# Performance work log

Measured on AMD Instinct MI355X. Metric: run time of the kernel, lower is better.

The kernel has to match this reference:

```python
import jax, jax.numpy as jnp
import numpy as np

B, T, K = 1024, 512, 64  # batch, max_seq_len, num_tags


def setup_inputs() -> dict:
    key = jax.random.key(0)
    k1, k2, k3, k4 = jax.random.split(key, 4)
    logits = jax.random.normal(k1, (B, T, K), dtype=jnp.float32)
    trans = jax.random.normal(k2, (K, K), dtype=jnp.float32) * 0.1  # self._crf_weights
    gold = jax.random.randint(k3, (B, T), 0, K)
    # training sentences contain at least 2 words (per the assignment comment)
    seq_len = jax.random.randint(k4, (B,), 2, T + 1)
    return {"logits": logits, "trans": trans, "gold": gold, "seq_len": seq_len}


def reference(logits, trans, gold, seq_len):
    # crf_loss: loss = -crf_log_likelihood(...) / batch_size
    Bsz, Tlen, _ = logits.shape
    pos = jnp.arange(Tlen)
    valid = pos[None, :] < seq_len[:, None]  # [B, T]

    # first_loss: sum of unary scores at gold tags over valid positions
    unary = jnp.take_along_axis(logits, gold[..., None], axis=2)[..., 0]  # [B, T]
    first = jnp.sum(jnp.where(valid, unary, 0.0))

    # second_loss: sum of transition scores trans[gold_t, gold_{t+1}] for t+1 < seq_len
    pair = trans[gold[:, :-1], gold[:, 1:]]  # [B, T-1]
    valid_pair = pos[None, :-1] < (seq_len - 1)[:, None]
    second = jnp.sum(jnp.where(valid_pair, pair, 0.0))

    # third_loss: log-partition via forward recurrence
    # alpha_new[a] = logsumexp_b(trans[a, b] + alpha[b]) + logits[:, t, a]
    # (note: source reduces over axis=1 of (trans + alpha), i.e. the second index)
    def step(alpha, xs):
        t, lt = xs  # lt: [B, K] logits at time t
        new = jax.nn.logsumexp(trans[None, :, :] + alpha[:, None, :], axis=2) + lt
        alpha = jnp.where((t < seq_len)[:, None], new, alpha)
        return alpha, None

    alpha0 = logits[:, 0, :]                         # [B, K]
    ts = jnp.arange(1, Tlen)
    rest = jnp.swapaxes(logits[:, 1:, :], 0, 1)      # [T-1, B, K]
    alpha_final, _ = jax.lax.scan(step, alpha0, (ts, rest))
    third = jnp.sum(jax.nn.logsumexp(alpha_final, axis=1))

    log_like = first + second - third
    return -log_like / Bsz
```

## Files before the change

kernel.cpp:

```cpp
#include <hip/hip_runtime.h>

#define BB 1024
#define TT 512
#define KK 64
#define CH 8

typedef _Float16 f16x2 __attribute__((ext_vector_type(2)));
typedef float f32x4 __attribute__((ext_vector_type(4)));
typedef unsigned int u32x4 __attribute__((ext_vector_type(4)));

__device__ __forceinline__ float wave_sum(float v) {
#pragma unroll
    for (int off = 1; off < 64; off <<= 1) v += __shfl_xor(v, off);
    return v;
}

__device__ __forceinline__ float wave_max(float v) {
#pragma unroll
    for (int off = 1; off < 64; off <<= 1) v = fmaxf(v, __shfl_xor(v, off));
    return v;
}

#if __has_builtin(__builtin_amdgcn_fdot2)
#define FDOT2(E, P, A) __builtin_amdgcn_fdot2((E), (P), (A), false)
#else
__device__ __forceinline__ float fdot2_emul(f16x2 e, f16x2 p, float a) {
    return fmaf((float)e.x, (float)p.x, fmaf((float)e.y, (float)p.y, a));
}
#define FDOT2(E, P, A) fdot2_emul((E), (P), (A))
#endif

__global__ void __launch_bounds__(64)
__attribute__((amdgpu_waves_per_eu(1, 1)))
crf_fwd(
    const float* __restrict__ logits,
    const float* __restrict__ trans,
    const int* __restrict__ gold,
    const int* __restrict__ seq_len,
    float* __restrict__ ws)
{
    __shared__ __align__(16) _Float16 plds[KK];
    const int b = blockIdx.x;
    const int j = threadIdx.x & 63;
    const float* lg = logits + (size_t)b * (TT * KK);
    const int* gd = gold + (size_t)b * TT;
    const int L = seq_len[b];

    float af = 0.0f, asec = 0.0f;
#pragma unroll
    for (int c = 0; c < TT / 64; ++c) {
        int t = c * 64 + j;
        if (t < L) {
            int g0 = gd[t];
            af += lg[t * KK + g0];
            if (t + 1 < L) {
                int g1 = gd[t + 1];
                asec += trans[g0 * KK + g1];
            }
        }
    }

    const float* Ej = trans + (size_t)j * KK;
#define DECLE(q) f16x2 Eh##q; { \
    float e0 = __expf(Ej[2 * (q)]); float e1 = __expf(Ej[2 * (q) + 1]); \
    Eh##q.x = (_Float16)e0; Eh##q.y = (_Float16)e1; }
    DECLE(0)  DECLE(1)  DECLE(2)  DECLE(3)  DECLE(4)  DECLE(5)  DECLE(6)  DECLE(7)
    DECLE(8)  DECLE(9)  DECLE(10) DECLE(11) DECLE(12) DECLE(13) DECLE(14) DECLE(15)
    DECLE(16) DECLE(17) DECLE(18) DECLE(19) DECLE(20) DECLE(21) DECLE(22) DECLE(23)
    DECLE(24) DECLE(25) DECLE(26) DECLE(27) DECLE(28) DECLE(29) DECLE(30) DECLE(31)
#undef DECLE

    float a0 = lg[j];
    float mx = wave_max(a0);
    float p0 = __expf(a0 - mx);
    _Float16 h0 = (_Float16)p0;
    float pq = (float)h0;
    plds[j] = h0;
    int Etot = 0;

    f32x4 nl0, nl1;
    nl0.x = lg[1 * KK + j]; nl0.y = lg[2 * KK + j];
    nl0.z = lg[3 * KK + j]; nl0.w = lg[4 * KK + j];
    nl1.x = lg[5 * KK + j]; nl1.y = lg[6 * KK + j];
    nl1.z = lg[7 * KK + j]; nl1.w = lg[8 * KK + j];

#define DOTQ(q, W, A) A = FDOT2(Eh##q, __builtin_bit_cast(f16x2, (W)), A);

#define STEP(ii, EL) { \
    const u32x4* pl4 = (const u32x4*)plds; \
    u32x4 R0 = pl4[0], R1 = pl4[1], R2 = pl4[2], R3 = pl4[3]; \
    u32x4 R4 = pl4[4], R5 = pl4[5], R6 = pl4[6], R7 = pl4[7]; \
    float A0 = 0.f, A1 = 0.f, A2 = 0.f, A3 = 0.f; \
    DOTQ(0,  R0.x, A0) DOTQ(1,  R0.y, A1) DOTQ(2,  R0.z, A2) DOTQ(3,  R0.w, A3) \
    DOTQ(4,  R1.x, A0) DOTQ(5,  R1.y, A1) DOTQ(6,  R1.z, A2) DOTQ(7,  R1.w, A3) \
    DOTQ(8,  R2.x, A0) DOTQ(9,  R2.y, A1) DOTQ(10, R2.z, A2) DOTQ(11, R2.w, A3) \
    DOTQ(12, R3.x, A0) DOTQ(13, R3.y, A1) DOTQ(14, R3.z, A2) DOTQ(15, R3.w, A3) \
    DOTQ(16, R4.x, A0) DOTQ(17, R4.y, A1) DOTQ(18, R4.z, A2) DOTQ(19, R4.w, A3) \
    DOTQ(20, R5.x, A0) DOTQ(21, R5.y, A1) DOTQ(22, R5.z, A2) DOTQ(23, R5.w, A3) \
    DOTQ(24, R6.x, A0) DOTQ(25, R6.y, A1) DOTQ(26, R6.z, A2) DOTQ(27, R6.w, A3) \
    DOTQ(28, R7.x, A0) DOTQ(29, R7.y, A1) DOTQ(30, R7.z, A2) DOTQ(31, R7.w, A3) \
    float s = (A0 + A1) + (A2 + A3); \
    float pn = s * (EL); \
    bool ok = (t0 + (ii)) < L; \
    pn = ok ? pn : pq; \
    unsigned sb = (unsigned)__builtin_amdgcn_readfirstlane((int)__float_as_uint(pn)); \
    int ee = ok ? ((int)((sb >> 23) & 255u) - 127) : 0; \
    Etot += ee; \
    float scl = __uint_as_float((unsigned)(127 - ee) << 23); \
    float qv = pn * scl; \
    _Float16 hq = (_Float16)qv; \
    pq = (float)hq; \
    plds[j] = hq; }

    for (int t0 = 1; t0 < L; t0 += CH) {
        asm volatile("" : "+v"(Eh0),  "+v"(Eh1),  "+v"(Eh2),  "+v"(Eh3),
                          "+v"(Eh4),  "+v"(Eh5),  "+v"(Eh6),  "+v"(Eh7),
                          "+v"(Eh8),  "+v"(Eh9),  "+v"(Eh10), "+v"(Eh11),
                          "+v"(Eh12), "+v"(Eh13), "+v"(Eh14), "+v"(Eh15));
        asm volatile("" : "+v"(Eh16), "+v"(Eh17), "+v"(Eh18), "+v"(Eh19),
                          "+v"(Eh20), "+v"(Eh21), "+v"(Eh22), "+v"(Eh23),
                          "+v"(Eh24), "+v"(Eh25), "+v"(Eh26), "+v"(Eh27),
                          "+v"(Eh28), "+v"(Eh29), "+v"(Eh30), "+v"(Eh31));

        f32x4 el0, el1;
        el0.x = __expf(nl0.x); el0.y = __expf(nl0.y);
        el0.z = __expf(nl0.z); el0.w = __expf(nl0.w);
        el1.x = __expf(nl1.x); el1.y = __expf(nl1.y);
        el1.z = __expf(nl1.z); el1.w = __expf(nl1.w);

        {
            int tn = t0 + CH;
            int c0 = tn + 0; c0 = (c0 > TT - 1) ? TT - 1 : c0;
            int c1 = tn + 1; c1 = (c1 > TT - 1) ? TT - 1 : c1;
            int c2 = tn + 2; c2 = (c2 > TT - 1) ? TT - 1 : c2;
            int c3 = tn + 3; c3 = (c3 > TT - 1) ? TT - 1 : c3;
            int c4 = tn + 4; c4 = (c4 > TT - 1) ? TT - 1 : c4;
            int c5 = tn + 5; c5 = (c5 > TT - 1) ? TT - 1 : c5;
            int c6 = tn + 6; c6 = (c6 > TT - 1) ? TT - 1 : c6;
            int c7 = tn + 7; c7 = (c7 > TT - 1) ? TT - 1 : c7;
            nl0.x = lg[c0 * KK + j]; nl0.y = lg[c1 * KK + j];
            nl0.z = lg[c2 * KK + j]; nl0.w = lg[c3 * KK + j];
            nl1.x = lg[c4 * KK + j]; nl1.y = lg[c5 * KK + j];
            nl1.z = lg[c6 * KK + j]; nl1.w = lg[c7 * KK + j];
        }

        STEP(0, el0.x) STEP(1, el0.y) STEP(2, el0.z) STEP(3, el0.w)
        STEP(4, el1.x) STEP(5, el1.y) STEP(6, el1.z) STEP(7, el1.w)
    }
#undef STEP
#undef DOTQ

    float sump = wave_sum(pq);
    float third_b = mx + (float)Etot * 0.6931471805599453f + __logf(sump);
    float first_b = wave_sum(af);
    float second_b = wave_sum(asec);

    if (j == 0) {
        ws[b] = (third_b - first_b - second_b) * (1.0f / (float)BB);
    }
}

__global__ void crf_reduce(const float* __restrict__ ws, float* __restrict__ out) {
    int tid = threadIdx.x;
    float v = ws[tid] + ws[tid + 256] + ws[tid + 512] + ws[tid + 768];
    v = wave_sum(v);
    __shared__ float sm[4];
    if ((tid & 63) == 0) sm[tid >> 6] = v;
    __syncthreads();
    if (tid == 0) out[0] = (sm[0] + sm[1]) + (sm[2] + sm[3]);
}

extern "C" void kernel_launch(void* const* d_in, const int* in_sizes, int n_in,
                              void* d_out, int out_size, void* d_ws, size_t ws_size,
                              hipStream_t stream) {
    const float* logits = (const float*)d_in[0];
    const float* trans  = (const float*)d_in[1];
    const int*   gold   = (const int*)d_in[2];
    const int*   slen   = (const int*)d_in[3];
    float* out = (float*)d_out;
    float* ws = (float*)d_ws;

    hipLaunchKernelGGL(crf_fwd, dim3(BB), dim3(64), 0, stream,
                       logits, trans, gold, slen, ws);
    hipLaunchKernelGGL(crf_reduce, dim3(1), dim3(256), 0, stream, ws, out);
}
```

Baseline: 103.6 us.

## Split matvec across lane quads with DPP reduction and peel the tail loop

Each lane now holds exp(trans) for four rows restricted to a 16-column slice, so each step reads only 32 bytes of the shared state vector instead of all 128. The per-row partial sums are combined across each quad of lanes with DPP xor-1 and xor-2 moves, replacing the previous full-row dot product per lane. The main loop now handles only full chunks of 8 steps, and a separate guarded tail handles the rest, which drops the per-step validity select and the register copy of the state. The aim is to cut LDS read traffic on the serial recurrence, at the cost of added cross-lane ops and select instructions on the critical path.

```diff
diff --git a/kernel.cpp b/kernel.cpp
--- a/kernel.cpp
+++ b/kernel.cpp
@@ -28,6 +28,20 @@
     return fmaf((float)e.x, (float)p.x, fmaf((float)e.y, (float)p.y, a));
 }
 #define FDOT2(E, P, A) fdot2_emul((E), (P), (A))
+#endif
+
+#if __has_builtin(__builtin_amdgcn_mov_dpp)
+__device__ __forceinline__ float dpp_xor1_f(float x) {
+    return __uint_as_float((unsigned)__builtin_amdgcn_mov_dpp(
+        (int)__float_as_uint(x), 0xB1, 0xF, 0xF, true));
+}
+__device__ __forceinline__ float dpp_xor2_f(float x) {
+    return __uint_as_float((unsigned)__builtin_amdgcn_mov_dpp(
+        (int)__float_as_uint(x), 0x4E, 0xF, 0xF, true));
+}
+#else
+__device__ __forceinline__ float dpp_xor1_f(float x) { return __shfl_xor(x, 1); }
+__device__ __forceinline__ float dpp_xor2_f(float x) { return __shfl_xor(x, 2); }
 #endif
 
 __global__ void __launch_bounds__(64)
@@ -46,6 +60,11 @@
     const int* gd = gold + (size_t)b * TT;
     const int L = seq_len[b];
 
+    const int quad_r = (j >> 2) << 2;
+    const int slice_c = (j & 3) << 4;
+    const bool lodd = (j & 1) != 0;
+    const bool lhi  = (j & 2) != 0;
+
     float af = 0.0f, asec = 0.0f;
 #pragma unroll
     for (int c = 0; c < TT / 64; ++c) {
@@ -60,22 +79,28 @@
         }
     }
 
-    const float* Ej = trans + (size_t)j * KK;
-#define DECLE(q) f16x2 Eh##q; { \
-    float e0 = __expf(Ej[2 * (q)]); float e1 = __expf(Ej[2 * (q) + 1]); \
-    Eh##q.x = (_Float16)e0; Eh##q.y = (_Float16)e1; }
-    DECLE(0)  DECLE(1)  DECLE(2)  DECLE(3)  DECLE(4)  DECLE(5)  DECLE(6)  DECLE(7)
-    DECLE(8)  DECLE(9)  DECLE(10) DECLE(11) DECLE(12) DECLE(13) DECLE(14) DECLE(15)
-    DECLE(16) DECLE(17) DECLE(18) DECLE(19) DECLE(20) DECLE(21) DECLE(22) DECLE(23)
-    DECLE(24) DECLE(25) DECLE(26) DECLE(27) DECLE(28) DECLE(29) DECLE(30) DECLE(31)
-#undef DECLE
+    f16x2 Eh0, Eh1, Eh2, Eh3, Eh4, Eh5, Eh6, Eh7;
+    f16x2 Eh8, Eh9, Eh10, Eh11, Eh12, Eh13, Eh14, Eh15;
+    f16x2 Eh16, Eh17, Eh18, Eh19, Eh20, Eh21, Eh22, Eh23;
+    f16x2 Eh24, Eh25, Eh26, Eh27, Eh28, Eh29, Eh30, Eh31;
+#define MKP(DST, a, bgt) { DST.x = (_Float16)__expf(a); DST.y = (_Float16)__expf(bgt); }
+#define DECROW(rr, N0, N1, N2, N3, N4, N5, N6, N7) { \
+    const float* row_ = trans + (size_t)(quad_r + (rr)) * KK + slice_c; \
+    f32x4 v0 = *(const f32x4*)(row_ + 0);  f32x4 v1 = *(const f32x4*)(row_ + 4); \
+    f32x4 v2 = *(const f32x4*)(row_ + 8);  f32x4 v3 = *(const f32x4*)(row_ + 12); \
+    MKP(N0, v0.x, v0.y) MKP(N1, v0.z, v0.w) MKP(N2, v1.x, v1.y) MKP(N3, v1.z, v1.w) \
+    MKP(N4, v2.x, v2.y) MKP(N5, v2.z, v2.w) MKP(N6, v3.x, v3.y) MKP(N7, v3.z, v3.w) }
+    DECROW(0, Eh0,  Eh1,  Eh2,  Eh3,  Eh4,  Eh5,  Eh6,  Eh7)
+    DECROW(1, Eh8,  Eh9,  Eh10, Eh11, Eh12, Eh13, Eh14, Eh15)
+    DECROW(2, Eh16, Eh17, Eh18, Eh19, Eh20, Eh21, Eh22, Eh23)
+    DECROW(3, Eh24, Eh25, Eh26, Eh27, Eh28, Eh29, Eh30, Eh31)
+#undef DECROW
+#undef MKP
 
     float a0 = lg[j];
     float mx = wave_max(a0);
     float p0 = __expf(a0 - mx);
-    _Float16 h0 = (_Float16)p0;
-    float pq = (float)h0;
-    plds[j] = h0;
+    plds[j] = (_Float16)p0;
     int Etot = 0;
 
     f32x4 nl0, nl1;
@@ -84,35 +109,38 @@
     nl1.x = lg[5 * KK + j]; nl1.y = lg[6 * KK + j];
     nl1.z = lg[7 * KK + j]; nl1.w = lg[8 * KK + j];
 
-#define DOTQ(q, W, A) A = FDOT2(Eh##q, __builtin_bit_cast(f16x2, (W)), A);
-
-#define STEP(ii, EL) { \
-    const u32x4* pl4 = (const u32x4*)plds; \
-    u32x4 R0 = pl4[0], R1 = pl4[1], R2 = pl4[2], R3 = pl4[3]; \
-    u32x4 R4 = pl4[4], R5 = pl4[5], R6 = pl4[6], R7 = pl4[7]; \
+    const u32x4* myslice = (const u32x4*)((const char*)plds + ((j & 3) << 5));
+
+#define DOTW(EH, W, A) A = FDOT2(EH, __builtin_bit_cast(f16x2, (W)), A);
+
+#define STEP(EL) { \
+    u32x4 Ra = myslice[0], Rb = myslice[1]; \
     float A0 = 0.f, A1 = 0.f, A2 = 0.f, A3 = 0.f; \
-    DOTQ(0,  R0.x, A0) DOTQ(1,  R0.y, A1) DOTQ(2,  R0.z, A2) DOTQ(3,  R0.w, A3) \
-    DOTQ(4,  R1.x, A0) DOTQ(5,  R1.y, A1) DOTQ(6,  R1.z, A2) DOTQ(7,  R1.w, A3) \
-    DOTQ(8,  R2.x, A0) DOTQ(9,  R2.y, A1) DOTQ(10, R2.z, A2) DOTQ(11, R2.w, A3) \
-    DOTQ(12, R3.x, A0) DOTQ(13, R3.y, A1) DOTQ(14, R3.z, A2) DOTQ(15, R3.w, A3) \
-    DOTQ(16, R4.x, A0) DOTQ(17, R4.y, A1) DOTQ(18, R4.z, A2) DOTQ(19, R4.w, A3) \
-    DOTQ(20, R5.x, A0) DOTQ(21, R5.y, A1) DOTQ(22, R5.z, A2) DOTQ(23, R5.w, A3) \
-    DOTQ(24, R6.x, A0) DOTQ(25, R6.y, A1) DOTQ(26, R6.z, A2) DOTQ(27, R6.w, A3) \
-    DOTQ(28, R7.x, A0) DOTQ(29, R7.y, A1) DOTQ(30, R7.z, A2) DOTQ(31, R7.w, A3) \
-    float s = (A0 + A1) + (A2 + A3); \
-    float pn = s * (EL); \
-    bool ok = (t0 + (ii)) < L; \
-    pn = ok ? pn : pq; \
+    float A4 = 0.f, A5 = 0.f, A6 = 0.f, A7 = 0.f; \
+    DOTW(Eh0,  Ra.x, A0) DOTW(Eh1,  Ra.y, A1) DOTW(Eh2,  Ra.z, A0) DOTW(Eh3,  Ra.w, A1) \
+    DOTW(Eh4,  Rb.x, A0) DOTW(Eh5,  Rb.y, A1) DOTW(Eh6,  Rb.z, A0) DOTW(Eh7,  Rb.w, A1) \
+    DOTW(Eh8,  Ra.x, A2) DOTW(Eh9,  Ra.y, A3) DOTW(Eh10, Ra.z, A2) DOTW(Eh11, Ra.w, A3) \
+    DOTW(Eh12, Rb.x, A2) DOTW(Eh13, Rb.y, A3) DOTW(Eh14, Rb.z, A2) DOTW(Eh15, Rb.w, A3) \
+    DOTW(Eh16, Ra.x, A4) DOTW(Eh17, Ra.y, A5) DOTW(Eh18, Ra.z, A4) DOTW(Eh19, Ra.w, A5) \
+    DOTW(Eh20, Rb.x, A4) DOTW(Eh21, Rb.y, A5) DOTW(Eh22, Rb.z, A4) DOTW(Eh23, Rb.w, A5) \
+    DOTW(Eh24, Ra.x, A6) DOTW(Eh25, Ra.y, A7) DOTW(Eh26, Ra.z, A6) DOTW(Eh27, Ra.w, A7) \
+    DOTW(Eh28, Rb.x, A6) DOTW(Eh29, Rb.y, A7) DOTW(Eh30, Rb.z, A6) DOTW(Eh31, Rb.w, A7) \
+    float P0 = A0 + A1, P1 = A2 + A3, P2 = A4 + A5, P3 = A6 + A7; \
+    float S0 = lodd ? P0 : P1, K0 = lodd ? P1 : P0; \
+    float S1 = lodd ? P2 : P3, K1 = lodd ? P3 : P2; \
+    float Q0 = K0 + dpp_xor1_f(S0); \
+    float Q1 = K1 + dpp_xor1_f(S1); \
+    float S2 = lhi ? Q0 : Q1, K2 = lhi ? Q1 : Q0; \
+    float s_ = K2 + dpp_xor2_f(S2); \
+    float pn = s_ * (EL); \
     unsigned sb = (unsigned)__builtin_amdgcn_readfirstlane((int)__float_as_uint(pn)); \
-    int ee = ok ? ((int)((sb >> 23) & 255u) - 127) : 0; \
+    int ee = (int)((sb >> 23) & 255u) - 127; \
     Etot += ee; \
-    float scl = __uint_as_float((unsigned)(127 - ee) << 23); \
-    float qv = pn * scl; \
-    _Float16 hq = (_Float16)qv; \
-    pq = (float)hq; \
-    plds[j] = hq; }
-
-    for (int t0 = 1; t0 < L; t0 += CH) {
+    float scl = __uint_as_float((unsigned)((127 - ee) << 23)); \
+    plds[j] = (_Float16)(pn * scl); }
+
+    int t0 = 1;
+    for (; t0 + CH <= L; t0 += CH) {
         asm volatile("" : "+v"(Eh0),  "+v"(Eh1),  "+v"(Eh2),  "+v"(Eh3),
                           "+v"(Eh4),  "+v"(Eh5),  "+v"(Eh6),  "+v"(Eh7),
                           "+v"(Eh8),  "+v"(Eh9),  "+v"(Eh10), "+v"(Eh11),
@@ -144,13 +172,29 @@
             nl1.z = lg[c6 * KK + j]; nl1.w = lg[c7 * KK + j];
         }
 
-        STEP(0, el0.x) STEP(1, el0.y) STEP(2, el0.z) STEP(3, el0.w)
-        STEP(4, el1.x) STEP(5, el1.y) STEP(6, el1.z) STEP(7, el1.w)
+        STEP(el0.x) STEP(el0.y) STEP(el0.z) STEP(el0.w)
+        STEP(el1.x) STEP(el1.y) STEP(el1.z) STEP(el1.w)
+    }
+
+    if (t0 < L) {
+        f32x4 el0, el1;
+        el0.x = __expf(nl0.x); el0.y = __expf(nl0.y);
+        el0.z = __expf(nl0.z); el0.w = __expf(nl0.w);
+        el1.x = __expf(nl1.x); el1.y = __expf(nl1.y);
+        el1.z = __expf(nl1.z); el1.w = __expf(nl1.w);
+        if (t0 + 0 < L) { STEP(el0.x) }
+        if (t0 + 1 < L) { STEP(el0.y) }
+        if (t0 + 2 < L) { STEP(el0.z) }
+        if (t0 + 3 < L) { STEP(el0.w) }
+        if (t0 + 4 < L) { STEP(el1.x) }
+        if (t0 + 5 < L) { STEP(el1.y) }
+        if (t0 + 6 < L) { STEP(el1.z) }
     }
 #undef STEP
-#undef DOTQ
-
-    float sump = wave_sum(pq);
+#undef DOTW
+
+    float pfin = (float)plds[j];
+    float sump = wave_sum(pfin);
     float third_b = mx + (float)Etot * 0.6931471805599453f + __logf(sump);
     float first_b = wave_sum(af);
     float second_b = wave_sum(asec);
```

After: 95.03 us. 8.3% less time.
